# Optimization experiments

Measured on AMD Instinct MI355X. Metric: run time of the kernel, lower is better.

The kernel has to match this reference:

```python
import jax, jax.numpy as jnp
import numpy as np

ANCHORS = np.array([[10,13],[16,30],[33,23],[30,61],[62,45],[59,119],[116,90],[156,198],[373,326]], np.float32)
SCALE = 2
STRIDE = [32, 16, 8][SCALE]
ANCH_MASK = [[6,7,8],[3,4,5],[0,1,2]][SCALE]
N_CLASSES = 91
IGNORE_THR = 0.5


def _bce(x, t):
    # BCEWithLogits, elementwise: softplus(x) - x*t
    return jax.nn.softplus(x) - x * t


def setup_inputs() -> dict:
    key = jax.random.key(0)
    k1, k2, k3, k4 = jax.random.split(key, 4)
    B, T, G = 16, 50, 64
    output = jax.random.normal(k1, (B, 3, G, G, 5 + N_CLASSES), dtype=jnp.float32) * 0.1
    cls = jax.random.randint(k2, (B, T), 0, N_CLASSES).astype(jnp.float32)
    xy = jax.random.uniform(k3, (B, T, 2), minval=0.05, maxval=0.95)
    wh = jax.random.uniform(k4, (B, T, 2), minval=0.02, maxval=0.4)
    labels = jnp.concatenate([cls[..., None], xy, wh], axis=-1)
    return {"output": output, "labels": labels}


def reference(output, labels):
    B, A, G = output.shape[0], output.shape[1], output.shape[2]
    n_ch = 5 + N_CLASSES
    all_grid = jnp.asarray(ANCHORS / STRIDE)                 # [9,2] anchors in grid units
    m_anch = all_grid[jnp.asarray(ANCH_MASK)]                # [3,2]

    # decoded predicted boxes (detached in original)
    gx = jnp.arange(G, dtype=output.dtype)
    p = jax.lax.stop_gradient(output)
    px = jax.nn.sigmoid(p[..., 0]) + gx[None, None, None, :]
    py = jax.nn.sigmoid(p[..., 1]) + gx[None, None, :, None]
    pw = jnp.exp(p[..., 2]) * m_anch[:, 0][None, :, None, None]
    ph = jnp.exp(p[..., 3]) * m_anch[:, 1][None, :, None, None]
    pred = jnp.stack([px, py, pw, ph], axis=-1).reshape(B, -1, 4)   # [B, N, 4], N = A*G*G

    tx = labels[:, :, 1] * G; ty = labels[:, :, 2] * G
    tw = labels[:, :, 3] * G; th = labels[:, :, 4] * G              # [B,T]
    valid = labels.sum(-1) > 0                                      # [B,T]

    # anchor IoU: truth (0,0,w,h) vs ref anchors (0,0,aw,ah)
    aw, ah = all_grid[:, 0], all_grid[:, 1]                         # [9]
    mw = jnp.minimum(tw[..., None], aw); mh = jnp.minimum(th[..., None], ah)
    inter_a = mw * mh * ((mw > 0) & (mh > 0))
    a_iou = inter_a / (tw[..., None] * th[..., None] + aw * ah - inter_a)   # [B,T,9]
    best_n_all = jnp.argmax(a_iou, axis=-1)
    best_n = best_n_all % 3
    in_scale = (best_n_all[..., None] == jnp.asarray(ANCH_MASK)).any(-1)
    mask_t = valid & in_scale                                       # [B,T] assigned targets

    # pred-vs-truth IoU (xywh) for ignore mask
    tb = jnp.stack([tx, ty, tw, th], axis=-1)                       # [B,T,4]
    tl = jnp.maximum(pred[:, :, None, :2] - pred[:, :, None, 2:] / 2,
                     tb[:, None, :, :2] - tb[:, None, :, 2:] / 2)
    br = jnp.minimum(pred[:, :, None, :2] + pred[:, :, None, 2:] / 2,
                     tb[:, None, :, :2] + tb[:, None, :, 2:] / 2)
    en = jnp.all(tl < br, axis=-1)
    area_i = jnp.prod(br - tl, axis=-1) * en
    area_p = pred[:, :, 2] * pred[:, :, 3]
    p_iou = area_i / (area_p[:, :, None] + (tw * th)[:, None, :] - area_i)  # [B,N,T]
    p_iou = jnp.where(valid[:, None, :], p_iou, 0.0)
    ignored = (p_iou.max(-1) > IGNORE_THR).reshape(B, A, G, G)
    obj_mask = (~ignored).astype(output.dtype)

    # scatter target assignments; invalid targets routed out-of-bounds (dropped)
    i_idx = tx.astype(jnp.int32); j_idx = ty.astype(jnp.int32)
    a_idx = best_n
    b_idx = jnp.broadcast_to(jnp.arange(B)[:, None], tx.shape)
    b_sc = jnp.where(mask_t, b_idx, B)

    obj_mask = obj_mask.at[b_sc, a_idx, j_idx, i_idx].set(1.0, mode='drop')
    tmask = jnp.zeros((B, A, G, G), output.dtype).at[b_sc, a_idx, j_idx, i_idx].set(1.0, mode='drop')
    tgt_scale = jnp.zeros((B, A, G, G), output.dtype).at[b_sc, a_idx, j_idx, i_idx].set(
        jnp.sqrt(2.0 - tw * th / (G * G)), mode='drop')

    target = jnp.zeros((B, A, G, G, n_ch), output.dtype)
    target = target.at[b_sc, a_idx, j_idx, i_idx, 0].set(tx - jnp.floor(tx), mode='drop')
    target = target.at[b_sc, a_idx, j_idx, i_idx, 1].set(ty - jnp.floor(ty), mode='drop')
    target = target.at[b_sc, a_idx, j_idx, i_idx, 2].set(jnp.log(tw / m_anch[a_idx, 0] + 1e-16), mode='drop')
    target = target.at[b_sc, a_idx, j_idx, i_idx, 3].set(jnp.log(th / m_anch[a_idx, 1] + 1e-16), mode='drop')
    target = target.at[b_sc, a_idx, j_idx, i_idx, 4].set(1.0, mode='drop')
    cls = labels[:, :, 0].astype(jnp.int32)
    target = target.at[b_sc, a_idx, j_idx, i_idx, 5 + cls].set(1.0, mode='drop')

    # masked losses (mask-weighted sums == boolean-gather + reduction='sum')
    loss_xy = jnp.sum(tmask[..., None] * _bce(output[..., 0:2], target[..., 0:2]))
    out_wh = output[..., 2:4] * tgt_scale[..., None]
    targ_wh = target[..., 2:4] * tgt_scale[..., None]
    loss_wh = jnp.sum(tmask[..., None] * (out_wh - targ_wh) ** 2) / 2
    loss_obj = jnp.sum(obj_mask * _bce(output[..., 4], target[..., 4]))
    loss_cls = jnp.sum(tmask[..., None] * _bce(output[..., 5:], target[..., 5:]))
    return loss_xy + loss_wh + loss_obj + loss_cls
```

## Files before the change

### kernel.cpp

```cpp
#include <hip/hip_runtime.h>
#include <math.h>

#define NT 50
#define NG 64
#define NCLS 91
#define NCH 96
#define CPB 128
#define CELL_BLOCKS 96
#define TGT_BLOCKS  13
#define BX (CELL_BLOCKS + TGT_BLOCKS)
#define NPART (BX * 16)

__device__ __constant__ float c_aw[9] = {1.25f, 2.0f, 4.125f, 3.75f, 7.75f, 7.375f, 14.5f, 19.5f, 46.625f};
__device__ __constant__ float c_ah[9] = {1.625f, 3.75f, 2.875f, 7.625f, 5.625f, 14.875f, 11.25f, 24.75f, 40.75f};

__device__ __forceinline__ float softplusf_fast(float x) {
    return __logf(1.0f + __expf(-fabsf(x))) + fmaxf(x, 0.0f);
}

__device__ __forceinline__ void target_match(float tw, float th, bool valid,
                                             float tx, float ty,
                                             bool& mask, int& cell, int& bn) {
    float area = tw * th;
    float best = -1.0f; int bna = 0;
    #pragma unroll
    for (int k = 0; k < 9; ++k) {
        float mw = fminf(tw, c_aw[k]);
        float mh = fminf(th, c_ah[k]);
        float inter = (mw > 0.0f && mh > 0.0f) ? mw * mh : 0.0f;
        float iou = inter / (area + c_aw[k] * c_ah[k] - inter);
        if (iou > best) { best = iou; bna = k; }
    }
    mask = valid && (bna < 3);
    bn = bna;
    cell = mask ? (bna * 4096 + ((int)ty) * 64 + (int)tx) : -1;
}

__global__ __launch_bounds__(256) void yolo_scale_loss_kernel(
        const float* __restrict__ outp, const float* __restrict__ lab,
        float* __restrict__ partials) {
    const int b    = blockIdx.y;
    const int tid  = threadIdx.x;
    const int lane = tid & 63;
    __shared__ float s_red[4];

    float contrib = 0.0f;

    if (blockIdx.x < CELL_BLOCKS) {
        __shared__ float4 s_box[NT];
        __shared__ float  s_area[NT];
        __shared__ unsigned char s_matched[CPB];

        const int cell_local = tid >> 1;
        const int half = tid & 1;
        const int blk_start = blockIdx.x * CPB;
        const int idx = blk_start + cell_local;
        const size_t base = ((size_t)b * 12288 + idx) * NCH;

        const float4 p03 = *(const float4*)(outp + base);
        const float  p4  = outp[base + 4];

        if (tid < CPB) s_matched[tid] = 0;
        if (tid < NT) {
            const float* L = lab + (size_t)(b * NT + tid) * 5;
            float cls = L[0], x = L[1], y = L[2], w = L[3], h = L[4];
            float tx = x * NG, ty = y * NG, tw = w * NG, th = h * NG;
            bool valid = (cls + x + y + w + h) > 0.0f;
            if (!valid) { tx = ty = tw = th = 0.0f; }
            bool mask; int cell, bn;
            target_match(tw, th, valid, tx, ty, mask, cell, bn);
            float hw = tw * 0.5f, hh = th * 0.5f;
            s_box[tid]  = make_float4(tx - hw, ty - hh, tx + hw, ty + hh);
            s_area[tid] = tw * th;
            if (cell >= blk_start && cell < blk_start + CPB)
                s_matched[cell - blk_start] = 1;
        }
        __syncthreads();

        const int a = idx >> 12;
        const int j = (idx >> 6) & 63;
        const int i = idx & 63;

        float pxc = 1.0f / (1.0f + __expf(-p03.x)) + (float)i;
        float pyc = 1.0f / (1.0f + __expf(-p03.y)) + (float)j;
        float pw  = __expf(p03.z) * c_aw[a];
        float ph  = __expf(p03.w) * c_ah[a];
        float parea = pw * ph;
        float pl = pxc - pw * 0.5f, pt = pyc - ph * 0.5f;
        float pr = pxc + pw * 0.5f, pb = pyc + ph * 0.5f;

        bool ign = false;
        const int t0 = half * 25;
        #pragma unroll 5
        for (int k = 0; k < 25; ++k) {
            float4 tb = s_box[t0 + k];
            float  ar = s_area[t0 + k];
            float tlx = fmaxf(pl, tb.x), tly = fmaxf(pt, tb.y);
            float brx = fminf(pr, tb.z), bry = fminf(pb, tb.w);
            float iw = brx - tlx, ih = bry - tly;
            float ai = iw * ih;
            ign = ign || ((fminf(iw, ih) > 0.0f) && (3.0f * ai > parea + ar));
        }
        int ign_i = ign ? 1 : 0;
        ign_i |= __shfl_xor(ign_i, 1, 64);

        if (half == 0) {
            bool matched = (s_matched[cell_local] != 0);
            contrib = matched ? (softplusf_fast(p4) - p4)
                              : (ign_i ? 0.0f : softplusf_fast(p4));
        }
    } else {
        const int t = (blockIdx.x - CELL_BLOCKS) * 4 + (tid >> 6);
        if (t < NT) {
            bool mask_l = false; int cell_l = -1, bn_l = 0, cls_l = 0;
            float txl = 0, tyl = 0, twl = 0, thl = 0;
            if (lane < NT) {
                const float* L = lab + (size_t)(b * NT + lane) * 5;
                float cls = L[0], x = L[1], y = L[2], w = L[3], h = L[4];
                txl = x * NG; tyl = y * NG; twl = w * NG; thl = h * NG;
                bool valid = (cls + x + y + w + h) > 0.0f;
                target_match(twl, thl, valid, txl, tyl, mask_l, cell_l, bn_l);
                cls_l = (int)cls;
            }
            const int cell_t = __shfl(cell_l, t);
            unsigned long long same = __ballot(mask_l && (cell_l == cell_t));
            bool winner = ((same >> t) & 1ull) &&
                          ((same & ((1ull << t) - 1ull)) == 0ull);
            if (winner) {
                const float tx = __shfl(txl, t), ty = __shfl(tyl, t);
                const float tw = __shfl(twl, t), th = __shfl(thl, t);
                const int   bn = __shfl(bn_l, t), cc = __shfl(cls_l, t);
                const size_t base = ((size_t)b * 12288 + cell_t) * NCH;

                float lsum = 0.0f;
                for (int c = lane; c < NCLS; c += 64) {
                    float pc = outp[base + 5 + c];
                    lsum += softplusf_fast(pc) - ((c == cc) ? pc : 0.0f);
                }
                if (lane == 0) {
                    float4 p03 = *(const float4*)(outp + base);
                    float tt0 = tx - floorf(tx), tt1 = ty - floorf(ty);
                    float tt2 = logf(tw / c_aw[bn] + 1e-16f);
                    float tt3 = logf(th / c_ah[bn] + 1e-16f);
                    float s2 = 2.0f - tw * th * (1.0f / (NG * NG));
                    lsum += softplusf_fast(p03.x) - p03.x * tt0;
                    lsum += softplusf_fast(p03.y) - p03.y * tt1;
                    float d2 = p03.z - tt2, d3 = p03.w - tt3;
                    lsum += 0.5f * s2 * (d2 * d2 + d3 * d3);
                }
                contrib = lsum;
            }
        }
    }

    float v = contrib;
    #pragma unroll
    for (int off = 32; off > 0; off >>= 1)
        v += __shfl_down(v, off, 64);
    if (lane == 0) s_red[tid >> 6] = v;
    __syncthreads();
    if (tid == 0)
        partials[blockIdx.y * BX + blockIdx.x] = s_red[0] + s_red[1] + s_red[2] + s_red[3];
}

__global__ __launch_bounds__(256) void final_reduce_kernel(
        const float* __restrict__ partials, float* __restrict__ out) {
    __shared__ float s_red[4];
    const int tid = threadIdx.x, lane = tid & 63;
    float v = 0.0f;
    for (int i = tid; i < NPART; i += 256) v += partials[i];
    #pragma unroll
    for (int off = 32; off > 0; off >>= 1)
        v += __shfl_down(v, off, 64);
    if (lane == 0) s_red[tid >> 6] = v;
    __syncthreads();
    if (tid == 0) out[0] = s_red[0] + s_red[1] + s_red[2] + s_red[3];
}

extern "C" void kernel_launch(void* const* d_in, const int* in_sizes, int n_in,
                              void* d_out, int out_size, void* d_ws, size_t ws_size,
                              hipStream_t stream) {
    const float* outp = (const float*)d_in[0];
    const float* lab  = (const float*)d_in[1];
    float* partials   = (float*)d_ws;
    float* res        = (float*)d_out;

    const int B = in_sizes[1] / (NT * 5);

    dim3 grid(BX, B);
    yolo_scale_loss_kernel<<<grid, 256, 0, stream>>>(outp, lab, partials);
    final_reduce_kernel<<<1, 256, 0, stream>>>(partials, res);
}
```

Baseline: 109.4 us.

## Cull truth boxes per block via bounding-box bound and fuse final reduction

Each cell block now handles one cell per thread and first computes a block-wide bounding box and the minimum predicted area. It uses these to build a compacted shared list of the truth boxes whose IoU could exceed the threshold, so each cell only tests that shortlist instead of all 50 truths. The separate final-reduce kernel is replaced by a last-block-done pattern using an atomic counter, with a memset added to reset the counter. The culling adds extra syncs and a shuffle reduction per block, and the atomic completion scheme adds a serialised tail in the last block.

```diff
diff --git a/kernel.cpp b/kernel.cpp
--- a/kernel.cpp
+++ b/kernel.cpp
@@ -5,8 +5,8 @@
 #define NG 64
 #define NCLS 91
 #define NCH 96
-#define CPB 128
-#define CELL_BLOCKS 96
+#define CPB 256
+#define CELL_BLOCKS 48
 #define TGT_BLOCKS  13
 #define BX (CELL_BLOCKS + TGT_BLOCKS)
 #define NPART (BX * 16)
@@ -38,29 +38,34 @@
 
 __global__ __launch_bounds__(256) void yolo_scale_loss_kernel(
         const float* __restrict__ outp, const float* __restrict__ lab,
-        float* __restrict__ partials) {
+        unsigned* __restrict__ counter, float* __restrict__ partials,
+        float* __restrict__ loss_out) {
     const int b    = blockIdx.y;
     const int tid  = threadIdx.x;
     const int lane = tid & 63;
+    const int wv   = tid >> 6;
     __shared__ float s_red[4];
+    __shared__ int   s_last;
 
     float contrib = 0.0f;
 
     if (blockIdx.x < CELL_BLOCKS) {
-        __shared__ float4 s_box[NT];
-        __shared__ float  s_area[NT];
+        __shared__ float4 s_boxF[NT];
+        __shared__ float  s_areaF[NT];
+        __shared__ float4 s_cbox[NT];
+        __shared__ float  s_carea[NT];
+        __shared__ float  s_wb[4][5];
+        __shared__ int    s_count;
         __shared__ unsigned char s_matched[CPB];
 
-        const int cell_local = tid >> 1;
-        const int half = tid & 1;
         const int blk_start = blockIdx.x * CPB;
-        const int idx = blk_start + cell_local;
+        const int idx = blk_start + tid;
         const size_t base = ((size_t)b * 12288 + idx) * NCH;
 
         const float4 p03 = *(const float4*)(outp + base);
         const float  p4  = outp[base + 4];
 
-        if (tid < CPB) s_matched[tid] = 0;
+        s_matched[tid] = 0;
         if (tid < NT) {
             const float* L = lab + (size_t)(b * NT + tid) * 5;
             float cls = L[0], x = L[1], y = L[2], w = L[3], h = L[4];
@@ -70,17 +75,15 @@
             bool mask; int cell, bn;
             target_match(tw, th, valid, tx, ty, mask, cell, bn);
             float hw = tw * 0.5f, hh = th * 0.5f;
-            s_box[tid]  = make_float4(tx - hw, ty - hh, tx + hw, ty + hh);
-            s_area[tid] = tw * th;
+            s_boxF[tid]  = make_float4(tx - hw, ty - hh, tx + hw, ty + hh);
+            s_areaF[tid] = tw * th;
             if (cell >= blk_start && cell < blk_start + CPB)
                 s_matched[cell - blk_start] = 1;
         }
-        __syncthreads();
 
         const int a = idx >> 12;
         const int j = (idx >> 6) & 63;
         const int i = idx & 63;
-
         float pxc = 1.0f / (1.0f + __expf(-p03.x)) + (float)i;
         float pyc = 1.0f / (1.0f + __expf(-p03.y)) + (float)j;
         float pw  = __expf(p03.z) * c_aw[a];
@@ -89,28 +92,61 @@
         float pl = pxc - pw * 0.5f, pt = pyc - ph * 0.5f;
         float pr = pxc + pw * 0.5f, pb = pyc + ph * 0.5f;
 
+        float BL = pl, BT = pt, BR = pr, BB = pb, PA = parea;
+        #pragma unroll
+        for (int off = 32; off > 0; off >>= 1) {
+            BL = fminf(BL, __shfl_xor(BL, off, 64));
+            BT = fminf(BT, __shfl_xor(BT, off, 64));
+            BR = fmaxf(BR, __shfl_xor(BR, off, 64));
+            BB = fmaxf(BB, __shfl_xor(BB, off, 64));
+            PA = fminf(PA, __shfl_xor(PA, off, 64));
+        }
+        if (lane == 0) {
+            s_wb[wv][0] = BL; s_wb[wv][1] = BT; s_wb[wv][2] = BR;
+            s_wb[wv][3] = BB; s_wb[wv][4] = PA;
+        }
+        __syncthreads();
+
+        if (wv == 0) {
+            float bl = fminf(fminf(s_wb[0][0], s_wb[1][0]), fminf(s_wb[2][0], s_wb[3][0]));
+            float bt = fminf(fminf(s_wb[0][1], s_wb[1][1]), fminf(s_wb[2][1], s_wb[3][1]));
+            float br = fmaxf(fmaxf(s_wb[0][2], s_wb[1][2]), fmaxf(s_wb[2][2], s_wb[3][2]));
+            float bb = fmaxf(fmaxf(s_wb[0][3], s_wb[1][3]), fmaxf(s_wb[2][3], s_wb[3][3]));
+            float pa = fminf(fminf(s_wb[0][4], s_wb[1][4]), fminf(s_wb[2][4], s_wb[3][4]));
+            bool keep = false;
+            float4 tb = make_float4(0, 0, 0, 0); float ar = 0.0f;
+            if (lane < NT) {
+                tb = s_boxF[lane]; ar = s_areaF[lane];
+                float iw = fminf(br, tb.z) - fmaxf(bl, tb.x);
+                float ih = fminf(bb, tb.w) - fmaxf(bt, tb.y);
+                float ai_ub = fmaxf(iw, 0.0f) * fmaxf(ih, 0.0f);
+                keep = (3.0f * ai_ub > pa + ar);
+            }
+            unsigned long long m = __ballot(keep);
+            if (keep) {
+                int pos = __popcll(m & ((1ull << lane) - 1ull));
+                s_cbox[pos]  = tb;
+                s_carea[pos] = ar;
+            }
+            if (lane == 0) s_count = __popcll(m);
+        }
+        __syncthreads();
+
+        const int cnt = s_count;
         bool ign = false;
-        const int t0 = half * 25;
-        #pragma unroll 5
-        for (int k = 0; k < 25; ++k) {
-            float4 tb = s_box[t0 + k];
-            float  ar = s_area[t0 + k];
-            float tlx = fmaxf(pl, tb.x), tly = fmaxf(pt, tb.y);
-            float brx = fminf(pr, tb.z), bry = fminf(pb, tb.w);
-            float iw = brx - tlx, ih = bry - tly;
+        for (int t = 0; t < cnt; ++t) {
+            float4 tb = s_cbox[t];
+            float  ar = s_carea[t];
+            float iw = fminf(pr, tb.z) - fmaxf(pl, tb.x);
+            float ih = fminf(pb, tb.w) - fmaxf(pt, tb.y);
             float ai = iw * ih;
             ign = ign || ((fminf(iw, ih) > 0.0f) && (3.0f * ai > parea + ar));
         }
-        int ign_i = ign ? 1 : 0;
-        ign_i |= __shfl_xor(ign_i, 1, 64);
-
-        if (half == 0) {
-            bool matched = (s_matched[cell_local] != 0);
-            contrib = matched ? (softplusf_fast(p4) - p4)
-                              : (ign_i ? 0.0f : softplusf_fast(p4));
-        }
+        bool matched = (s_matched[tid] != 0);
+        contrib = matched ? (softplusf_fast(p4) - p4)
+                          : (ign ? 0.0f : softplusf_fast(p4));
     } else {
-        const int t = (blockIdx.x - CELL_BLOCKS) * 4 + (tid >> 6);
+        const int t = (blockIdx.x - CELL_BLOCKS) * 4 + wv;
         if (t < NT) {
             bool mask_l = false; int cell_l = -1, bn_l = 0, cls_l = 0;
             float txl = 0, tyl = 0, twl = 0, thl = 0;
@@ -157,24 +193,33 @@
     #pragma unroll
     for (int off = 32; off > 0; off >>= 1)
         v += __shfl_down(v, off, 64);
-    if (lane == 0) s_red[tid >> 6] = v;
+    if (lane == 0) s_red[wv] = v;
     __syncthreads();
-    if (tid == 0)
-        partials[blockIdx.y * BX + blockIdx.x] = s_red[0] + s_red[1] + s_red[2] + s_red[3];
-}
-
-__global__ __launch_bounds__(256) void final_reduce_kernel(
-        const float* __restrict__ partials, float* __restrict__ out) {
-    __shared__ float s_red[4];
-    const int tid = threadIdx.x, lane = tid & 63;
-    float v = 0.0f;
-    for (int i = tid; i < NPART; i += 256) v += partials[i];
-    #pragma unroll
-    for (int off = 32; off > 0; off >>= 1)
-        v += __shfl_down(v, off, 64);
-    if (lane == 0) s_red[tid >> 6] = v;
+    if (tid == 0) {
+        float p = s_red[0] + s_red[1] + s_red[2] + s_red[3];
+        const int gid = blockIdx.y * BX + blockIdx.x;
+        __hip_atomic_store(&partials[gid], p, __ATOMIC_RELEASE,
+                           __HIP_MEMORY_SCOPE_AGENT);
+        unsigned old = __hip_atomic_fetch_add(counter, 1u, __ATOMIC_ACQ_REL,
+                                              __HIP_MEMORY_SCOPE_AGENT);
+        s_last = (old == NPART - 1) ? 1 : 0;
+    }
     __syncthreads();
-    if (tid == 0) out[0] = s_red[0] + s_red[1] + s_red[2] + s_red[3];
+
+    if (s_last) {
+        float v2 = 0.0f;
+        for (int k = tid; k < NPART; k += 256)
+            v2 += __hip_atomic_load(&partials[k], __ATOMIC_ACQUIRE,
+                                    __HIP_MEMORY_SCOPE_AGENT);
+        #pragma unroll
+        for (int off = 32; off > 0; off >>= 1)
+            v2 += __shfl_down(v2, off, 64);
+        __syncthreads();
+        if (lane == 0) s_red[wv] = v2;
+        __syncthreads();
+        if (tid == 0)
+            loss_out[0] = s_red[0] + s_red[1] + s_red[2] + s_red[3];
+    }
 }
 
 extern "C" void kernel_launch(void* const* d_in, const int* in_sizes, int n_in,
@@ -182,12 +227,13 @@
                               hipStream_t stream) {
     const float* outp = (const float*)d_in[0];
     const float* lab  = (const float*)d_in[1];
-    float* partials   = (float*)d_ws;
+    unsigned* counter = (unsigned*)d_ws;
+    float* partials   = (float*)((char*)d_ws + 256);
     float* res        = (float*)d_out;
 
     const int B = in_sizes[1] / (NT * 5);
 
+    hipMemsetAsync(counter, 0, sizeof(unsigned), stream);
     dim3 grid(BX, B);
-    yolo_scale_loss_kernel<<<grid, 256, 0, stream>>>(outp, lab, partials);
-    final_reduce_kernel<<<1, 256, 0, stream>>>(partials, res);
-}
+    yolo_scale_loss_kernel<<<grid, 256, 0, stream>>>(outp, lab, counter, partials, res);
+}
```

After: 141.8 us. +29.6%, slower.
